# Performance work log

Measured on AMD Instinct MI355X. Metric: run time of the kernel, lower is better.

## Reference

```python
import jax, jax.numpy as jnp
import numpy as np

BN, S, D = 200, 128, 1024          # B*N entity rows, scenes, d_model
D_INNER, D_STATE, D_CONV = 2048, 32, 4


def setup_inputs() -> dict:
    key = jax.random.key(0)
    ks = jax.random.split(key, 8)
    s = 0.02
    return {
        "x": jax.random.normal(ks[0], (BN, S, D), jnp.float32),
        "emotion_bias": jax.random.uniform(ks[1], (BN, S, 1), jnp.float32),
        "norm_w": jnp.ones((D,), jnp.float32),
        "norm_b": jnp.zeros((D,), jnp.float32),
        "in_proj_W": jax.random.normal(ks[2], (2 * D_INNER, D), jnp.float32) * s,
        "conv_w": jax.random.normal(ks[3], (D_INNER, 1, D_CONV), jnp.float32) * 0.1,
        "conv_b": jnp.zeros((D_INNER,), jnp.float32),
        "x_proj_W": jax.random.normal(ks[4], (2 * D_STATE + 1, D_INNER), jnp.float32) * s,
        "dt_W": jax.random.normal(ks[5], (D_INNER, 1), jnp.float32),
        "dt_b": jnp.zeros((D_INNER,), jnp.float32),
        "out_W": jax.random.normal(ks[6], (D, D_INNER), jnp.float32) * s,
        "emotion_scale": jnp.array(0.1, jnp.float32),
    }


def reference(x, emotion_bias, norm_w, norm_b, in_proj_W, conv_w, conv_b,
              x_proj_W, dt_W, dt_b, out_W, emotion_scale):
    residual = x
    # LayerNorm (eps=1e-5, biased variance as in torch)
    mu = x.mean(-1, keepdims=True)
    var = ((x - mu) ** 2).mean(-1, keepdims=True)
    xn = (x - mu) * jax.lax.rsqrt(var + 1e-5) * norm_w + norm_b

    xz = xn @ in_proj_W.T                      # [BN, S, 2*d_inner]
    x_in, z = jnp.split(xz, 2, axis=-1)

    # causal depthwise conv1d (torch pads d_conv-1 both sides, truncates to S == left-pad only)
    xc = jax.lax.conv_general_dilated(
        x_in.transpose(0, 2, 1), conv_w,
        window_strides=(1,), padding=[(D_CONV - 1, 0)],
        feature_group_count=D_INNER,
        dimension_numbers=("NCH", "OIH", "NCH"))
    xc = (xc + conv_b[None, :, None]).transpose(0, 2, 1)   # [BN, S, d_inner]
    x_act = jax.nn.silu(xc)

    x_ssm = x_act @ x_proj_W.T                 # [BN, S, 2*d_state+1]
    delta_raw, B_mat, C = jnp.split(x_ssm, [1, 1 + D_STATE], axis=-1)
    delta = jax.nn.softplus(delta_raw @ dt_W.T + dt_b)     # [BN, S, d_inner]
    delta = jnp.maximum(delta + emotion_scale * emotion_bias, 1e-4)

    def step(h, inp):
        d_t, B_t, C_t, xa_t = inp              # [BN,d_inner],[BN,n],[BN,n],[BN,d_inner]
        h = h * jnp.exp(-d_t)[..., None] + B_t[:, None, :] * xa_t[..., None]
        h = jnp.clip(h, -100.0, 100.0)
        y_t = jnp.einsum("bdn,bn->bd", h, C_t)
        return h, y_t

    h0 = jnp.zeros((BN, D_INNER, D_STATE), jnp.float32)
    xs = (delta.transpose(1, 0, 2), B_mat.transpose(1, 0, 2),
          C.transpose(1, 0, 2), x_act.transpose(1, 0, 2))
    _, y = jax.lax.scan(step, h0, xs)          # y: [S, BN, d_inner]
    y = y.transpose(1, 0, 2)

    return (y * jax.nn.silu(z)) @ out_W.T + residual
```

## Files before the change

kernel.cpp:

```cpp
#include <hip/hip_runtime.h>
#include <cstdint>
#include <cstddef>

#define NBN   200
#define NS    128
#define ND    1024
#define NDI   2048
#define NST   32
#define NROWS (NBN * NS)

typedef __attribute__((ext_vector_type(8))) short bf16x8;
typedef __attribute__((ext_vector_type(4))) float f32x4;

__device__ __forceinline__ unsigned short f2bf(float f) {
    unsigned int u = __float_as_uint(f);
    u += 0x7fffu + ((u >> 16) & 1u);
    return (unsigned short)(u >> 16);
}
__device__ __forceinline__ float bf2f(unsigned short h) {
    return __uint_as_float(((unsigned int)h) << 16);
}

__device__ __forceinline__ void gl_lds16(const void* g, void* l) {
    typedef __attribute__((address_space(1))) const unsigned int* gp_t;
    typedef __attribute__((address_space(3))) unsigned int* lp_t;
    __builtin_amdgcn_global_load_lds((gp_t)(uintptr_t)g,
                                     (lp_t)(unsigned int)(uintptr_t)l, 16, 0, 0);
}

__global__ __launch_bounds__(256) void cvt_kernel(const float* __restrict__ src,
                                                  unsigned short* __restrict__ dst, int n) {
    int i = blockIdx.x * 256 + threadIdx.x;
    if (i < n) dst[i] = f2bf(src[i]);
}

__global__ __launch_bounds__(256) void padwx_kernel(const float* __restrict__ src,
                                                    unsigned short* __restrict__ dst) {
    int i = blockIdx.x * 256 + threadIdx.x;
    int r = i >> 11;
    dst[i] = (r < 65) ? f2bf(src[i]) : (unsigned short)0;
}

__global__ __launch_bounds__(256) void ln_kernel(const float* __restrict__ x,
                                                 const float* __restrict__ gw,
                                                 const float* __restrict__ gb,
                                                 unsigned short* __restrict__ xn) {
    __shared__ float ss[4], ss2[4];
    size_t row = blockIdx.x;
    int tid = threadIdx.x;
    const float4* px = (const float4*)(x + row * ND);
    float4 v = px[tid];
    float s  = v.x + v.y + v.z + v.w;
    float s2 = fmaf(v.x, v.x, fmaf(v.y, v.y, fmaf(v.z, v.z, v.w * v.w)));
    #pragma unroll
    for (int off = 32; off > 0; off >>= 1) {
        s  += __shfl_down(s,  off, 64);
        s2 += __shfl_down(s2, off, 64);
    }
    if ((tid & 63) == 0) { ss[tid >> 6] = s; ss2[tid >> 6] = s2; }
    __syncthreads();
    float tot  = ss[0] + ss[1] + ss[2] + ss[3];
    float tot2 = ss2[0] + ss2[1] + ss2[2] + ss2[3];
    float mu   = tot * (1.f / ND);
    float var  = fmaf(tot2, 1.f / ND, -mu * mu);
    float rstd = rsqrtf(var + 1e-5f);
    float4 wv = ((const float4*)gw)[tid];
    float4 bv = ((const float4*)gb)[tid];
    ushort4 o;
    o.x = f2bf(fmaf((v.x - mu) * rstd, wv.x, bv.x));
    o.y = f2bf(fmaf((v.y - mu) * rstd, wv.y, bv.y));
    o.z = f2bf(fmaf((v.z - mu) * rstd, wv.z, bv.z));
    o.w = f2bf(fmaf((v.w - mu) * rstd, wv.w, bv.w));
    ((ushort4*)(xn + row * ND))[tid] = o;
}


#define BARRIER __builtin_amdgcn_s_barrier()
#define LGKM0  asm volatile("s_waitcnt lgkmcnt(0)" ::: "memory")
#define VMCNT6 asm volatile("s_waitcnt vmcnt(6)" ::: "memory")
#define VMCNT0 asm volatile("s_waitcnt vmcnt(0)" ::: "memory")
#define NOWAIT ((void)0)
#define PRIO1  __builtin_amdgcn_s_setprio(1)
#define PRIO0  __builtin_amdgcn_s_setprio(0)

#define STG_A(t, kp) {                                                        \
    gl_lds16(gA0 + (size_t)(t) * 64 + (kp) * 32,                              \
             lA + (((t) & 1) << 15) + ((kp) << 14));                          \
    gl_lds16(gA1 + (size_t)(t) * 64 + (kp) * 32,                              \
             lA + (((t) & 1) << 15) + ((kp) << 14) + 8192); }
#define STG_B(t, kp) {                                                        \
    gl_lds16(gB0 + (size_t)(t) * 64 + (kp) * 32,                              \
             lB + (((t) & 1) << 15) + ((kp) << 14));                          \
    gl_lds16(gB1 + (size_t)(t) * 64 + (kp) * 32,                              \
             lB + (((t) & 1) << 15) + ((kp) << 14) + 8192); }

#define RD_A(dst, mh, kp) { _Pragma("unroll")                                 \
    for (int mi = 0; mi < 4; ++mi)                                            \
        dst[mi] = *(const bf16x8*)(aRd + bo + (kp) * 16384 + (mh) * 4096 + mi * 1024); }
#define RD_B(dst, kp) { _Pragma("unroll")                                     \
    for (int ni = 0; ni < 4; ++ni)                                            \
        dst[ni] = *(const bf16x8*)(bRd + bo + (kp) * 16384 + ni * 1024); }

#define MM(mh, AV, BV) { _Pragma("unroll")                                    \
    for (int mi = 0; mi < 4; ++mi) { _Pragma("unroll")                        \
        for (int ni = 0; ni < 4; ++ni)                                        \
            acc[(mh) * 4 + mi][ni] = __builtin_amdgcn_mfma_f32_16x16x32_bf16( \
                AV[mi], BV[ni], acc[(mh) * 4 + mi][ni], 0, 0, 0); } }

#define TILE(t, DO_AP1, DO_T2, W) {                                           \
    const int bo = ((t) & 1) << 15;                                           \
    RD_A(aK0, 0, 0); RD_B(bK0, 0);                                            \
    if (DO_AP1) STG_A((t) + 1, 1);                                            \
    BARRIER; LGKM0; PRIO1; MM(0, aK0, bK0); PRIO0; BARRIER;                   \
    RD_A(aK1, 0, 1); RD_B(bK1, 1);                                            \
    if (DO_T2) STG_B((t) + 2, 0);                                             \
    BARRIER; LGKM0; PRIO1; MM(0, aK1, bK1); PRIO0; BARRIER;                   \
    RD_A(aK0, 1, 0);                                                          \
    if (DO_T2) STG_B((t) + 2, 1);                                             \
    BARRIER; LGKM0; PRIO1; MM(1, aK0, bK0); PRIO0; BARRIER;                   \
    RD_A(aK1, 1, 1);                                                          \
    if (DO_T2) STG_A((t) + 2, 0);                                             \
    BARRIER; LGKM0; PRIO1; MM(1, aK1, bK1); PRIO0;                            \
    W;                                                                        \
    BARRIER; }

template <int K, int EPI>
__global__ __launch_bounds__(512, 2)
void gemm256(const unsigned short* __restrict__ A,
             const unsigned short* __restrict__ B,
             int N, void* __restrict__ outp, const float* __restrict__ resid,
             const float* __restrict__ cw, const float* __restrict__ cb,
             unsigned short* __restrict__ out2) {
    constexpr int NT = K / 64;
    static_assert(NT >= 3, "need >=3 K-tiles");
    __shared__ __align__(16) char smem[131072];

    const int tid  = threadIdx.x;
    const int lane = tid & 63;
    const int wid  = tid >> 6;
    const int lrow = lane & 15;
    const int kq   = lane >> 4;
    const int wmi  = wid >> 2;
    const int wni  = wid & 3;

    const int gx  = gridDim.x;
    const int gy  = gridDim.y;
    const int nwg = gx * gy;
    const int lin = blockIdx.y * gx + blockIdx.x;
    const int id2 = (lin & 7) * (nwg >> 3) + (lin >> 3);
    const int bn  = id2 % gy;
    const int bm  = id2 / gy;

    const size_t m0 = (size_t)bm * 256;
    const size_t n0 = (size_t)bn * 256;

    const int fr = (lrow >> 1) & 3;
    const char* aRd = smem +          (wmi * 128 + lrow) * 64 + ((kq ^ fr) << 4);
    const char* bRd = smem + 65536 + (wni * 64  + lrow) * 64 + ((kq ^ fr) << 4);

    const int srow = wid * 16 + (lane >> 2);
    const int scol = (((lane & 3) ^ ((lane >> 3) & 3)) << 3);
    const unsigned short* gA0 = A + (m0 + srow) * K + scol;
    const unsigned short* gA1 = A + (m0 + 128 + srow) * K + scol;
    const unsigned short* gB0 = B + (n0 + srow) * K + scol;
    const unsigned short* gB1 = B + (n0 + 128 + srow) * K + scol;
    char* lA = smem + wid * 1024;
    char* lB = smem + 65536 + wid * 1024;

    f32x4 acc[8][4];
    #pragma unroll
    for (int i = 0; i < 8; ++i)
        #pragma unroll
        for (int j = 0; j < 4; ++j) acc[i][j] = (f32x4){0.f, 0.f, 0.f, 0.f};

    bf16x8 aK0[4], aK1[4], bK0[4], bK1[4];

    STG_B(0, 0); STG_B(0, 1); STG_A(0, 0); STG_A(0, 1);
    STG_B(1, 0); STG_B(1, 1); STG_A(1, 0);
    VMCNT6;
    BARRIER;

    int t = 0;
    #pragma unroll 2
    for (; t < NT - 2; ++t) { TILE(t, 1, 1, VMCNT6); }
    TILE((NT - 2), 1, 0, VMCNT0);
    TILE((NT - 1), 0, 0, NOWAIT);

    if (EPI == 1) {
        #pragma unroll
        for (int mi = 0; mi < 8; ++mi)
            #pragma unroll
            for (int ni = 0; ni < 4; ++ni)
                #pragma unroll
                for (int r = 0; r < 4; ++r) {
                    size_t row = m0 + wmi * 128 + mi * 16 + kq * 4 + r;
                    size_t col = n0 + wni * 64 + ni * 16 + lrow;
                    size_t idx = row * (size_t)N + col;
                    float v = acc[mi][ni][r] + __builtin_nontemporal_load(&resid[idx]);
                    __builtin_nontemporal_store(v, &((float*)outp)[idx]);
                }
    } else {
        BARRIER;
        if (n0 < 2048) {
            char* wb = smem + wid * 16384;
            #pragma unroll
            for (int mi = 0; mi < 8; ++mi)
                #pragma unroll
                for (int ni = 0; ni < 4; ++ni) {
                    int cl = ni * 16 + lrow;
                    int slot = mi * 2 + (kq >> 1);
                    ushort4 pk;
                    pk.x = f2bf(acc[mi][ni][0]); pk.y = f2bf(acc[mi][ni][1]);
                    pk.z = f2bf(acc[mi][ni][2]); pk.w = f2bf(acc[mi][ni][3]);
                    *(ushort4*)(wb + cl * 256 +
                                (((slot ^ lrow) << 4) | ((kq & 1) << 3))) = pk;
                }
            LGKM0;
            __builtin_amdgcn_sched_barrier(0);
            const int ch = (int)n0 + wni * 64 + lane;
            float4 wv = ((const float4*)cw)[ch];
            float bias = cb[ch];
            float x0 = 0.f, x1 = 0.f, x2 = 0.f;
            unsigned short* po = (unsigned short*)outp + (m0 + wmi * 128) * NDI + ch;
            const char* rb = wb + lane * 256;
            const int cx = lane & 15;
            for (int s = 0; s < 16; ++s) {
                bf16x8 v = *(const bf16x8*)(rb + ((s ^ cx) << 4));
                #pragma unroll
                for (int j = 0; j < 8; ++j) {
                    float x3 = bf2f((unsigned short)v[j]);
                    float vv = fmaf(x3, wv.w, fmaf(x2, wv.z,
                               fmaf(x1, wv.y, fmaf(x0, wv.x, bias))));
                    float sg = vv * __builtin_amdgcn_rcpf(1.f + __expf(-vv));
                    po[(size_t)(s * 8 + j) * NDI] = f2bf(sg);
                    x0 = x1; x1 = x2; x2 = x3;
                }
            }
        } else {
            #pragma unroll
            for (int mi = 0; mi < 8; ++mi)
                #pragma unroll
                for (int ni = 0; ni < 4; ++ni)
                    #pragma unroll
                    for (int r = 0; r < 4; ++r) {
                        size_t row = m0 + wmi * 128 + mi * 16 + kq * 4 + r;
                        size_t col = (n0 - 2048) + wni * 64 + ni * 16 + lrow;
                        float v = acc[mi][ni][r];
                        float sg = v * __builtin_amdgcn_rcpf(1.f + __expf(-v));
                        out2[row * 2048 + col] = f2bf(sg);
                    }
        }
    }
}

__global__ __launch_bounds__(256, 2)
void gemm2_kernel(const unsigned short* __restrict__ A,
                  const unsigned short* __restrict__ B,
                  float* __restrict__ out) {
    __shared__ __align__(16) unsigned short As[64 * 32];
    __shared__ __align__(16) unsigned short Bs[80 * 32];
    const int tid  = threadIdx.x;
    const int bm   = blockIdx.x;
    const int wid  = tid >> 6;
    const int lane = tid & 63;
    const int lrow = lane & 15;
    const int kq   = lane >> 4;

    f32x4 acc[5];
    #pragma unroll
    for (int i = 0; i < 5; i++) acc[i] = (f32x4){0.f, 0.f, 0.f, 0.f};

    const int r1 = tid >> 2;
    const int c8 = (tid & 3) << 3;
    const unsigned short* gA1 = A + ((size_t)bm * 64 + r1) * NDI + c8;
    const unsigned short* gB1 = B + (size_t)r1 * NDI + c8;
    const unsigned short* gB2 = B + (size_t)(64 + r1) * NDI + c8;
    char* lA1 = (char*)As + wid * 1024;
    char* lB1 = (char*)Bs + wid * 1024;
    char* lB2 = (char*)Bs + 4096;

    for (int kt = 0; kt < NDI; kt += 32) {
        __syncthreads();
        gl_lds16(gA1, lA1);
        gl_lds16(gB1, lB1);
        if (tid < 64) gl_lds16(gB2, lB2);
        gA1 += 32; gB1 += 32; gB2 += 32;
        __syncthreads();
        bf16x8 af = *(const bf16x8*)&As[(wid * 16 + lrow) * 32 + kq * 8];
        #pragma unroll
        for (int ni = 0; ni < 5; ni++) {
            bf16x8 bfr = *(const bf16x8*)&Bs[(ni * 16 + lrow) * 32 + kq * 8];
            acc[ni] = __builtin_amdgcn_mfma_f32_16x16x32_bf16(af, bfr, acc[ni], 0, 0, 0);
        }
    }
    #pragma unroll
    for (int ni = 0; ni < 5; ni++)
        #pragma unroll
        for (int r = 0; r < 4; r++) {
            size_t row = (size_t)bm * 64 + wid * 16 + kq * 4 + r;
            int col = ni * 16 + lrow;
            out[row * 80 + col] = acc[ni][r];
        }
}

__global__ __launch_bounds__(256, 2)
void ssd_kernel(const float* __restrict__ xssm,
                unsigned short* xact_g,
                const unsigned short* __restrict__ zs,
                const float* __restrict__ dtW,
                const float* __restrict__ dtb,
                const float* __restrict__ eb,
                const float* __restrict__ es_p) {
    __shared__ float sDR[32], sDE[32];
    __shared__ __align__(16) unsigned short sC[32][32];
    __shared__ __align__(16) unsigned short sB[32][32];
    __shared__ __align__(16) unsigned short sBt[32][32];
    __shared__ __align__(16) unsigned short sG[32][32];
    __shared__ __align__(16) unsigned short sP[256][32];
    __shared__ __align__(16) float          sE[256][32];
    __shared__ __align__(16) unsigned short sH[256][32];

    const int tid  = threadIdx.x;
    const int b    = blockIdx.y;
    const int d0   = blockIdx.x * 256;
    const int lane = tid & 63;
    const int wid  = tid >> 6;
    const int lrow = lane & 15;
    const int kq   = lane >> 4;
    const int wd0  = wid * 64;

    const float w  = dtW[d0 + tid];
    const float bb = dtb[d0 + tid];
    const float es = es_p[0];

    for (int i = tid; i < 256 * 32; i += 256) ((unsigned short*)sH)[i] = 0;

    #pragma unroll 1
    for (int c = 0; c < 4; ++c) {
        __syncthreads();
        {
            const float* src = xssm + ((size_t)b * 128 + c * 32) * 80;
            for (int i = tid; i < 2560; i += 256) {
                int t = i / 80, col = i - t * 80;
                float v = src[i];
                if (col == 0) sDR[t] = v;
                else if (col < 33) {
                    unsigned short bv = f2bf(v);
                    sB[t][col - 1] = bv;
                    sBt[col - 1][t] = bv;
                } else if (col < 65) sC[t][col - 33] = f2bf(v);
            }
            if (tid < 32) sDE[tid] = es * eb[b * 128 + c * 32 + tid];
        }
        __syncthreads();

        {
            int mi = wid >> 1, ni = wid & 1;
            bf16x8 af = *(const bf16x8*)&sC[mi * 16 + lrow][kq * 8];
            bf16x8 bf = *(const bf16x8*)&sB[ni * 16 + lrow][kq * 8];
            f32x4 z4 = (f32x4){0.f, 0.f, 0.f, 0.f};
            f32x4 g = __builtin_amdgcn_mfma_f32_16x16x32_bf16(af, bf, z4, 0, 0, 0);
            #pragma unroll
            for (int r = 0; r < 4; ++r) {
                int t = mi * 16 + kq * 4 + r, s = ni * 16 + lrow;
                float val = (s <= t) ? g[r] : 0.f;
                *(unsigned short*)((char*)sG + t * 64 +
                    ((((s >> 3) ^ (t & 3)) << 4) | ((s & 7) << 1))) = f2bf(val);
            }
        }

        {
            const unsigned short* pxa =
                xact_g + ((size_t)b * 128 + c * 32) * 2048 + d0 + tid;
            float L = 0.f;
            for (int t8 = 0; t8 < 4; ++t8) {
                bf16x8 pv;
                #pragma unroll
                for (int j = 0; j < 8; ++j) {
                    int t = t8 * 8 + j;
                    float raw = fmaf(sDR[t], w, bb);
                    float sp  = (raw > 20.f) ? raw : __logf(1.f + __expf(raw));
                    float delta = fmaxf(sp + sDE[t], 1e-4f);
                    L += delta;
                    float xa = bf2f(pxa[(size_t)t * 2048]);
                    pv[j] = (short)f2bf(xa * __expf(L));
                    *(float*)((char*)sE + tid * 128 +
                        ((((t >> 2) ^ (tid & 7)) << 4) | ((t & 3) << 2))) = __expf(-L);
                }
                *(bf16x8*)((char*)sP + tid * 64 + (((t8 ^ (tid & 3)) << 4))) = pv;
            }
        }
        __syncthreads();

        f32x4 acc[2][4], racc[2][4];
        bf16x8 cfrag[2], gfrag[2], btfrag[2], hfrag[4], pfrag[4];
        #pragma unroll
        for (int mi = 0; mi < 2; ++mi) {
            int tr = mi * 16 + lrow;
            cfrag[mi]  = *(const bf16x8*)&sC[tr][kq * 8];
            gfrag[mi]  = *(const bf16x8*)((const char*)sG + tr * 64 +
                                          (((kq ^ (tr & 3)) << 4)));
            btfrag[mi] = *(const bf16x8*)&sBt[tr][kq * 8];
        }
        #pragma unroll
        for (int ni = 0; ni < 4; ++ni) {
            int dc = wd0 + ni * 16 + lrow;
            hfrag[ni] = *(const bf16x8*)&sH[dc][kq * 8];
            pfrag[ni] = *(const bf16x8*)((const char*)sP + dc * 64 +
                                         (((kq ^ (dc & 3)) << 4)));
        }
        #pragma unroll
        for (int mi = 0; mi < 2; ++mi)
            #pragma unroll
            for (int ni = 0; ni < 4; ++ni) {
                f32x4 z4 = (f32x4){0.f, 0.f, 0.f, 0.f};
                acc[mi][ni] = __builtin_amdgcn_mfma_f32_16x16x32_bf16(
                    cfrag[mi], hfrag[ni], z4, 0, 0, 0);
                acc[mi][ni] = __builtin_amdgcn_mfma_f32_16x16x32_bf16(
                    gfrag[mi], pfrag[ni], acc[mi][ni], 0, 0, 0);
                racc[mi][ni] = __builtin_amdgcn_mfma_f32_16x16x32_bf16(
                    btfrag[mi], pfrag[ni], z4, 0, 0, 0);
            }

        #pragma unroll
        for (int mi = 0; mi < 2; ++mi)
            #pragma unroll
            for (int ni = 0; ni < 4; ++ni) {
                int dc = wd0 + ni * 16 + lrow;
                f32x4 ev = *(const f32x4*)((const char*)sE + dc * 128 +
                                           ((((mi * 4 + kq) ^ (dc & 7)) << 4)));
                size_t rowg = (size_t)b * 128 + c * 32 + mi * 16 + kq * 4;
                #pragma unroll
                for (int r = 0; r < 4; ++r) {
                    size_t gi = (rowg + r) * 2048 + d0 + dc;
                    float y  = acc[mi][ni][r] * ev[r];
                    xact_g[gi] = f2bf(y * bf2f(zs[gi]));
                }
            }

        #pragma unroll
        for (int ni = 0; ni < 4; ++ni) {
            int dc = wd0 + ni * 16 + lrow;
            float e31 = *(const float*)((const char*)sE + dc * 128 +
                                        (((7 ^ (dc & 7)) << 4) | 12));
            #pragma unroll
            for (int mi = 0; mi < 2; ++mi)
                #pragma unroll
                for (int r = 0; r < 4; ++r) {
                    int n = mi * 16 + kq * 4 + r;
                    float h = bf2f(sH[dc][n]) + racc[mi][ni][r];
                    sH[dc][n] = f2bf(e31 * h);
                }
        }
    }
}

extern "C" void kernel_launch(void* const* d_in, const int* in_sizes, int n_in,
                              void* d_out, int out_size, void* d_ws, size_t ws_size,
                              hipStream_t stream) {
    const float* x   = (const float*)d_in[0];
    const float* eb  = (const float*)d_in[1];
    const float* nw  = (const float*)d_in[2];
    const float* nb  = (const float*)d_in[3];
    const float* Wi  = (const float*)d_in[4];
    const float* cw  = (const float*)d_in[5];
    const float* cb  = (const float*)d_in[6];
    const float* Wx  = (const float*)d_in[7];
    const float* dtW = (const float*)d_in[8];
    const float* dtb = (const float*)d_in[9];
    const float* Wo  = (const float*)d_in[10];
    const float* es  = (const float*)d_in[11];
    float* out = (float*)d_out;

    char* ws = (char*)d_ws;
    unsigned short* wi_b   = (unsigned short*)(ws + 0);
    unsigned short* wo_b   = (unsigned short*)(ws + 8388608);
    unsigned short* wx_b   = (unsigned short*)(ws + 12582912);
    unsigned short* zs_b   = (unsigned short*)(ws + 12910592);
    unsigned short* xn_b   = (unsigned short*)(ws + 117768192);
    unsigned short* xact_b = (unsigned short*)(ws + 170196992);
    float*          xssm   = (float*)(ws + 275054592);
    if (ws_size < (size_t)283246592) return;

    cvt_kernel<<<(2 * NDI * ND + 255) / 256, 256, 0, stream>>>(Wi, wi_b, 2 * NDI * ND);
    cvt_kernel<<<(ND * NDI + 255) / 256, 256, 0, stream>>>(Wo, wo_b, ND * NDI);
    padwx_kernel<<<(80 * NDI) / 256, 256, 0, stream>>>(Wx, wx_b);

    ln_kernel<<<NROWS, 256, 0, stream>>>(x, nw, nb, xn_b);

    gemm256<ND, 2><<<dim3(NROWS / 256, (2 * NDI) / 256), 512, 0, stream>>>(
        xn_b, wi_b, 2 * NDI, xact_b, nullptr, cw, cb, zs_b);

    gemm2_kernel<<<NROWS / 64, 256, 0, stream>>>(xact_b, wx_b, xssm);

    ssd_kernel<<<dim3(NDI / 256, NBN), 256, 0, stream>>>(xssm, xact_b, zs_b, dtW, dtb, eb, es);

    gemm256<NDI, 1><<<dim3(NROWS / 256, ND / 256), 512, 0, stream>>>(
        xact_b, wo_b, ND, out, x, nullptr, nullptr, nullptr);
}
```

Before: 811.3 us.

## Software-pipeline SSD chunk loads into registers and overlap with compute

Unrolls the four-chunk SSD loop into macro bodies that prefetch the next chunk's x_ssm row, emotion bias and x_act column into registers while the current chunk computes, staging them to shared memory after a barrier. It also splits the cumulative-decay computation into a parallel softplus pass plus a serial prefix sum, and replaces exp(-L) with a reciprocal of exp(L). The aim is to hide global-load latency and cut a barrier per chunk, at the cost of many more live registers (two 32-element x_act buffers) under launch_bounds(256,2), which could spill or lower occupancy.

```diff
diff --git a/kernel.cpp b/kernel.cpp
--- a/kernel.cpp
+++ b/kernel.cpp
@@ -303,6 +303,151 @@
         }
 }
 
+#define SSD_PF(c, XN) {                                                       \
+    const float* src = xssm + ((size_t)b * 128 + ((c) + 1) * 32) * 80;        \
+    _Pragma("unroll")                                                         \
+    for (int k = 0; k < 10; ++k) fr[k] = src[tid + k * 256];                  \
+    ebr = (tid < 32) ? es * eb[b * 128 + ((c) + 1) * 32 + tid] : 0.f;         \
+    const unsigned short* pxa =                                               \
+        xact_g + ((size_t)b * 128 + ((c) + 1) * 32) * 2048 + d0 + tid;        \
+    _Pragma("unroll")                                                         \
+    for (int t = 0; t < 32; ++t) XN[t] = pxa[(size_t)t * 2048];               \
+}
+
+#define SSD_WSTG() {                                                          \
+    _Pragma("unroll")                                                         \
+    for (int k = 0; k < 10; ++k) {                                            \
+        int i = tid + k * 256;                                                \
+        int t = i / 80, col = i - t * 80;                                     \
+        float v = fr[k];                                                      \
+        if (col == 0) sDR[t] = v;                                             \
+        else if (col < 33) { unsigned short bv = f2bf(v);                     \
+            sB[t][col - 1] = bv; sBt[col - 1][t] = bv; }                      \
+        else if (col < 65) sC[t][col - 33] = f2bf(v);                         \
+    }                                                                         \
+    if (tid < 32) sDE[tid] = ebr;                                             \
+}
+
+#define SSD_BODY(c, XC, XN, DOPF) {                                           \
+    if (DOPF) SSD_PF(c, XN)                          \
+                    \
+    {                                                                         \
+        int gmi = wid >> 1, gni = wid & 1;                                    \
+        bf16x8 af = *(const bf16x8*)&sC[gmi * 16 + lrow][kq * 8];             \
+        bf16x8 bv = *(const bf16x8*)&sB[gni * 16 + lrow][kq * 8];             \
+        f32x4 z4 = (f32x4){0.f, 0.f, 0.f, 0.f};                               \
+        f32x4 g = __builtin_amdgcn_mfma_f32_16x16x32_bf16(af, bv, z4, 0,0,0); \
+        _Pragma("unroll")                                                     \
+        for (int r = 0; r < 4; ++r) {                                         \
+            int t = gmi * 16 + kq * 4 + r, s = gni * 16 + lrow;               \
+            float val = (s <= t) ? g[r] : 0.f;                                \
+            *(unsigned short*)((char*)sG + t * 64 +                           \
+                ((((s >> 3) ^ (t & 3)) << 4) | ((s & 7) << 1))) = f2bf(val);  \
+        }                                                                     \
+    }                                                                         \
+                             \
+    {                                                                         \
+        float L[32];                                                          \
+        _Pragma("unroll")                                                     \
+        for (int t = 0; t < 32; ++t) {                                        \
+            float raw = fmaf(sDR[t], w, bb);                                  \
+            float sp  = (raw > 20.f) ? raw : __logf(1.f + __expf(raw));       \
+            L[t] = fmaxf(sp + sDE[t], 1e-4f);                                 \
+        }                                                                     \
+        _Pragma("unroll")                                                     \
+        for (int t = 1; t < 32; ++t) L[t] += L[t - 1];                        \
+        _Pragma("unroll")                                                     \
+        for (int t8 = 0; t8 < 4; ++t8) {                                      \
+            bf16x8 pv;                                                        \
+            _Pragma("unroll")                                                 \
+            for (int j = 0; j < 8; ++j) {                                     \
+                int t = t8 * 8 + j;                                           \
+                float E = __expf(L[t]);                                       \
+                pv[j] = (short)f2bf(bf2f(XC[t]) * E);                         \
+                *(float*)((char*)sE + tid * 128 +                             \
+                    ((((t >> 2) ^ (tid & 7)) << 4) | ((t & 3) << 2))) =       \
+                    __builtin_amdgcn_rcpf(E);                                 \
+            }                                                                 \
+            *(bf16x8*)((char*)sP + tid * 64 + (((t8 ^ (tid & 3)) << 4))) = pv;\
+        }                                                                     \
+    }                                                                         \
+                  \
+    f32x4 acc[2][4], racc[2][4];                                              \
+    bf16x8 gfrag[2], pfrag[4];                                                \
+    {                                                                         \
+        bf16x8 cfrag[2], btfrag[2], hfrag[4];                                 \
+        _Pragma("unroll")                                                     \
+        for (int mi = 0; mi < 2; ++mi) {                                      \
+            int tr = mi * 16 + lrow;                                          \
+            cfrag[mi]  = *(const bf16x8*)&sC[tr][kq * 8];                     \
+            btfrag[mi] = *(const bf16x8*)&sBt[tr][kq * 8];                    \
+        }                                                                     \
+        _Pragma("unroll")                                                     \
+        for (int ni = 0; ni < 4; ++ni) {                                      \
+            int dc = wd0 + ni * 16 + lrow;                                    \
+            hfrag[ni] = *(const bf16x8*)&sH[dc][kq * 8];                      \
+            pfrag[ni] = *(const bf16x8*)((const char*)sP + dc * 64 +          \
+                                         (((kq ^ (dc & 3)) << 4)));           \
+        }                                                                     \
+        _Pragma("unroll")                                                     \
+        for (int mi = 0; mi < 2; ++mi)                                        \
+            _Pragma("unroll")                                                 \
+            for (int ni = 0; ni < 4; ++ni) {                                  \
+                f32x4 z4 = (f32x4){0.f, 0.f, 0.f, 0.f};                       \
+                acc[mi][ni] = __builtin_amdgcn_mfma_f32_16x16x32_bf16(        \
+                    cfrag[mi], hfrag[ni], z4, 0, 0, 0);                       \
+                racc[mi][ni] = __builtin_amdgcn_mfma_f32_16x16x32_bf16(       \
+                    btfrag[mi], pfrag[ni], z4, 0, 0, 0);                      \
+            }                                                                 \
+    }                                                                         \
+    __syncthreads();                              \
+    if (DOPF) SSD_WSTG()                          \
+    _Pragma("unroll")                                                         \
+    for (int mi = 0; mi < 2; ++mi) {                                          \
+        int tr = mi * 16 + lrow;                                              \
+        gfrag[mi] = *(const bf16x8*)((const char*)sG + tr * 64 +              \
+                                     (((kq ^ (tr & 3)) << 4)));               \
+    }                                                                         \
+    _Pragma("unroll")                                                         \
+    for (int mi = 0; mi < 2; ++mi)                                            \
+        _Pragma("unroll")                                                     \
+        for (int ni = 0; ni < 4; ++ni)                                        \
+            acc[mi][ni] = __builtin_amdgcn_mfma_f32_16x16x32_bf16(            \
+                gfrag[mi], pfrag[ni], acc[mi][ni], 0, 0, 0);                  \
+                                   \
+    _Pragma("unroll")                                                         \
+    for (int mi = 0; mi < 2; ++mi)                                            \
+        _Pragma("unroll")                                                     \
+        for (int ni = 0; ni < 4; ++ni) {                                      \
+            int dc = wd0 + ni * 16 + lrow;                                    \
+            f32x4 ev = *(const f32x4*)((const char*)sE + dc * 128 +           \
+                                       ((((mi * 4 + kq) ^ (dc & 7)) << 4)));  \
+            size_t rowg = (size_t)b * 128 + (c) * 32 + mi * 16 + kq * 4;      \
+            _Pragma("unroll")                                                 \
+            for (int r = 0; r < 4; ++r) {                                     \
+                size_t gi = (rowg + r) * 2048 + d0 + dc;                      \
+                float y  = acc[mi][ni][r] * ev[r];                            \
+                xact_g[gi] = f2bf(y * bf2f(zs[gi]));                          \
+            }                                                                 \
+        }                                                                     \
+                      \
+    _Pragma("unroll")                                                         \
+    for (int ni = 0; ni < 4; ++ni) {                                          \
+        int dc = wd0 + ni * 16 + lrow;                                        \
+        float e31 = *(const float*)((const char*)sE + dc * 128 +              \
+                                    (((7 ^ (dc & 7)) << 4) | 12));            \
+        _Pragma("unroll")                                                     \
+        for (int mi = 0; mi < 2; ++mi)                                        \
+            _Pragma("unroll")                                                 \
+            for (int r = 0; r < 4; ++r) {                                     \
+                int n = mi * 16 + kq * 4 + r;                                 \
+                float h = bf2f(sH[dc][n]) + racc[mi][ni][r];                  \
+                sH[dc][n] = f2bf(e31 * h);                                    \
+            }                                                                 \
+    }                                                                         \
+    __syncthreads();                                                          \
+}
+
 __global__ __launch_bounds__(256, 2)
 void ssd_kernel(const float* __restrict__ xssm,
                 unsigned short* xact_g,
@@ -335,124 +480,25 @@
 
     for (int i = tid; i < 256 * 32; i += 256) ((unsigned short*)sH)[i] = 0;
 
-    #pragma unroll 1
-    for (int c = 0; c < 4; ++c) {
-        __syncthreads();
-        {
-            const float* src = xssm + ((size_t)b * 128 + c * 32) * 80;
-            for (int i = tid; i < 2560; i += 256) {
-                int t = i / 80, col = i - t * 80;
-                float v = src[i];
-                if (col == 0) sDR[t] = v;
-                else if (col < 33) {
-                    unsigned short bv = f2bf(v);
-                    sB[t][col - 1] = bv;
-                    sBt[col - 1][t] = bv;
-                } else if (col < 65) sC[t][col - 33] = f2bf(v);
-            }
-            if (tid < 32) sDE[tid] = es * eb[b * 128 + c * 32 + tid];
-        }
-        __syncthreads();
-
-        {
-            int mi = wid >> 1, ni = wid & 1;
-            bf16x8 af = *(const bf16x8*)&sC[mi * 16 + lrow][kq * 8];
-            bf16x8 bf = *(const bf16x8*)&sB[ni * 16 + lrow][kq * 8];
-            f32x4 z4 = (f32x4){0.f, 0.f, 0.f, 0.f};
-            f32x4 g = __builtin_amdgcn_mfma_f32_16x16x32_bf16(af, bf, z4, 0, 0, 0);
-            #pragma unroll
-            for (int r = 0; r < 4; ++r) {
-                int t = mi * 16 + kq * 4 + r, s = ni * 16 + lrow;
-                float val = (s <= t) ? g[r] : 0.f;
-                *(unsigned short*)((char*)sG + t * 64 +
-                    ((((s >> 3) ^ (t & 3)) << 4) | ((s & 7) << 1))) = f2bf(val);
-            }
-        }
-
-        {
-            const unsigned short* pxa =
-                xact_g + ((size_t)b * 128 + c * 32) * 2048 + d0 + tid;
-            float L = 0.f;
-            for (int t8 = 0; t8 < 4; ++t8) {
-                bf16x8 pv;
-                #pragma unroll
-                for (int j = 0; j < 8; ++j) {
-                    int t = t8 * 8 + j;
-                    float raw = fmaf(sDR[t], w, bb);
-                    float sp  = (raw > 20.f) ? raw : __logf(1.f + __expf(raw));
-                    float delta = fmaxf(sp + sDE[t], 1e-4f);
-                    L += delta;
-                    float xa = bf2f(pxa[(size_t)t * 2048]);
-                    pv[j] = (short)f2bf(xa * __expf(L));
-                    *(float*)((char*)sE + tid * 128 +
-                        ((((t >> 2) ^ (tid & 7)) << 4) | ((t & 3) << 2))) = __expf(-L);
-                }
-                *(bf16x8*)((char*)sP + tid * 64 + (((t8 ^ (tid & 3)) << 4))) = pv;
-            }
-        }
-        __syncthreads();
-
-        f32x4 acc[2][4], racc[2][4];
-        bf16x8 cfrag[2], gfrag[2], btfrag[2], hfrag[4], pfrag[4];
+    float fr[10]; float ebr;
+    unsigned short xaA[32], xaB[32];
+
+    {
+        const float* src = xssm + ((size_t)b * 128) * 80;
         #pragma unroll
-        for (int mi = 0; mi < 2; ++mi) {
-            int tr = mi * 16 + lrow;
-            cfrag[mi]  = *(const bf16x8*)&sC[tr][kq * 8];
-            gfrag[mi]  = *(const bf16x8*)((const char*)sG + tr * 64 +
-                                          (((kq ^ (tr & 3)) << 4)));
-            btfrag[mi] = *(const bf16x8*)&sBt[tr][kq * 8];
-        }
+        for (int k = 0; k < 10; ++k) fr[k] = src[tid + k * 256];
+        ebr = (tid < 32) ? es * eb[b * 128 + tid] : 0.f;
+        const unsigned short* pxa = xact_g + ((size_t)b * 128) * 2048 + d0 + tid;
         #pragma unroll
-        for (int ni = 0; ni < 4; ++ni) {
-            int dc = wd0 + ni * 16 + lrow;
-            hfrag[ni] = *(const bf16x8*)&sH[dc][kq * 8];
-            pfrag[ni] = *(const bf16x8*)((const char*)sP + dc * 64 +
-                                         (((kq ^ (dc & 3)) << 4)));
-        }
-        #pragma unroll
-        for (int mi = 0; mi < 2; ++mi)
-            #pragma unroll
-            for (int ni = 0; ni < 4; ++ni) {
-                f32x4 z4 = (f32x4){0.f, 0.f, 0.f, 0.f};
-                acc[mi][ni] = __builtin_amdgcn_mfma_f32_16x16x32_bf16(
-                    cfrag[mi], hfrag[ni], z4, 0, 0, 0);
-                acc[mi][ni] = __builtin_amdgcn_mfma_f32_16x16x32_bf16(
-                    gfrag[mi], pfrag[ni], acc[mi][ni], 0, 0, 0);
-                racc[mi][ni] = __builtin_amdgcn_mfma_f32_16x16x32_bf16(
-                    btfrag[mi], pfrag[ni], z4, 0, 0, 0);
-            }
-
-        #pragma unroll
-        for (int mi = 0; mi < 2; ++mi)
-            #pragma unroll
-            for (int ni = 0; ni < 4; ++ni) {
-                int dc = wd0 + ni * 16 + lrow;
-                f32x4 ev = *(const f32x4*)((const char*)sE + dc * 128 +
-                                           ((((mi * 4 + kq) ^ (dc & 7)) << 4)));
-                size_t rowg = (size_t)b * 128 + c * 32 + mi * 16 + kq * 4;
-                #pragma unroll
-                for (int r = 0; r < 4; ++r) {
-                    size_t gi = (rowg + r) * 2048 + d0 + dc;
-                    float y  = acc[mi][ni][r] * ev[r];
-                    xact_g[gi] = f2bf(y * bf2f(zs[gi]));
-                }
-            }
-
-        #pragma unroll
-        for (int ni = 0; ni < 4; ++ni) {
-            int dc = wd0 + ni * 16 + lrow;
-            float e31 = *(const float*)((const char*)sE + dc * 128 +
-                                        (((7 ^ (dc & 7)) << 4) | 12));
-            #pragma unroll
-            for (int mi = 0; mi < 2; ++mi)
-                #pragma unroll
-                for (int r = 0; r < 4; ++r) {
-                    int n = mi * 16 + kq * 4 + r;
-                    float h = bf2f(sH[dc][n]) + racc[mi][ni][r];
-                    sH[dc][n] = f2bf(e31 * h);
-                }
-        }
+        for (int t = 0; t < 32; ++t) xaA[t] = pxa[(size_t)t * 2048];
+        SSD_WSTG()
     }
+    __syncthreads();
+
+    SSD_BODY(0, xaA, xaB, 1)
+    SSD_BODY(1, xaB, xaA, 1)
+    SSD_BODY(2, xaA, xaB, 1)
+    SSD_BODY(3, xaB, xaA, 0)
 }
 
 extern "C" void kernel_launch(void* const* d_in, const int* in_sizes, int n_in,
```

Result: slower. 830.8 us (+2.4%).
